# Kernel optimization log

Measured on AMD Instinct MI355X. Metric: run time of the kernel, lower is better.

Reference implementation:

```python
import jax, jax.numpy as jnp
import numpy as np

D = 768      # embed_dim
L = 8        # depth
NH = 4       # num_heads
HD = D // NH # head_dim = 192
GS = 16      # grid size (max_grid_size)
S = GS * GS  # 256 tokens
B = 64
EPS = 1.1920929e-07  # torch.finfo(float32).eps (RMSNorm eps=None)


def rmsnorm(x):
    return x * jax.lax.rsqrt(jnp.mean(x * x, axis=-1, keepdims=True) + EPS)


def householder_Q(vs):
    # sequential chain of Householder reflections: Q <- Q - (2/||v||^2) v (v^T Q)
    def step(Q, v):
        v = v[:, None]
        Q = Q - (2.0 / (jnp.sum(v * v) + 1e-08)) * (v @ (v.T @ Q))
        return Q, None
    Q, _ = jax.lax.scan(step, jnp.eye(vs.shape[1], dtype=vs.dtype), vs)
    return Q


def setup_inputs() -> dict:
    key = jax.random.key(0)
    ks = jax.random.split(key, 16)
    r = lambda k, shape, s=0.02: jax.random.normal(k, shape, jnp.float32) * s
    return dict(
        z_t=jax.random.normal(ks[0], (B, 3, 32, 32), jnp.float32),
        logsnr=jax.random.normal(ks[1], (B,), jnp.float32),
        qkv_w=r(ks[2], (L, D, 3 * D)),
        out_w=r(ks[3], (L, D, D)),
        gate_w=r(ks[4], (L, D, D)), gate_b=jnp.zeros((L, D), jnp.float32),
        mlpg_w=r(ks[5], (L, D, 8 * D)), mlpg_b=jnp.zeros((L, 8 * D), jnp.float32),
        mlpo_w=r(ks[6], (L, 4 * D, D)), mlpo_b=jnp.zeros((L, D), jnp.float32),
        hh_vs=r(ks[7], (L, HD // 2, HD)),
        patch_w=r(ks[8], (20, D)), patch_b=jnp.zeros((D,), jnp.float32),
        head_w=r(ks[9], (D, 12)), head_b=jnp.zeros((12,), jnp.float32),
        sd1_w=r(ks[10], (8, D)), sd1_b=jnp.zeros((D,), jnp.float32),
        sd2_w=r(ks[11], (D, 12)), sd2_b=jnp.zeros((12,), jnp.float32),
        lam_w=r(ks[12], (D, 1)), lam_b=jnp.zeros((1,), jnp.float32),
    )


def reference(z_t, logsnr, qkv_w, out_w, gate_w, gate_b, mlpg_w, mlpg_b,
              mlpo_w, mlpo_b, hh_vs, patch_w, patch_b, head_w, head_b,
              sd1_w, sd1_b, sd2_w, sd2_b, lam_w, lam_b):
    Bn, C, Him, Wim = z_t.shape
    gh = Him // 2
    # patchify 2x2 -> [B, S, 12]
    patches = z_t.reshape(Bn, C, gh, 2, gh, 2).transpose(0, 2, 4, 1, 3, 5).reshape(Bn, S, 12)
    # FourierFeatures(num_bands=4) -> 8-dim sin/cos embedding of logsnr
    bands = 2.0 ** jnp.arange(4, dtype=jnp.float32)
    ang = logsnr[:, None] * bands
    spins = jnp.concatenate([jnp.sin(ang), jnp.cos(ang)], axis=-1)  # [B, 8]
    x = jnp.concatenate([patches, jnp.broadcast_to(spins[:, None, :], (Bn, S, 8))], axis=-1) @ patch_w + patch_b

    # 2D RoPE tables on the 16x16 grid
    yy, xx = jnp.meshgrid(jnp.arange(GS), jnp.arange(GS), indexing='ij')
    coords = jnp.stack([yy.ravel(), xx.ravel()], axis=1).astype(jnp.float32)  # [S, 2]
    dim_half = HD // 2
    inv_freq = 1.0 / 10000.0 ** (jnp.arange(0, dim_half, 2, dtype=jnp.float32) / dim_half)
    fy = coords[:, 0:1] * inv_freq
    fx = coords[:, 1:2] * inv_freq
    emb = jnp.concatenate([fy, fx, fy, fx], axis=-1)  # [S, HD]
    cos, sin = jnp.cos(emb), jnp.sin(emb)

    # local sliding-window mask: euclidean distance on grid < 2.5
    d2 = jnp.sum((coords[:, None, :] - coords[None, :, :]) ** 2, axis=-1)
    local_mask = d2 < 2.5 ** 2  # [S, S]
    is_glob = jnp.array([(i + 1) % 4 == 0 for i in range(L)])
    scale = 1.0 / jnp.sqrt(jnp.float32(HD))

    def layer(x, p):
        qw, ow, gw, gb, mgw, mgb, mow, mob, vs, glob = p
        h = rmsnorm(x)
        q, k, v = jnp.split(h @ qw, 3, axis=-1)
        heads = lambda t: t.reshape(Bn, S, NH, HD).transpose(0, 2, 1, 3)  # [B,H,S,hd]
        q, k, v = heads(q), heads(k), heads(v)
        # RnRoPE: inverse Householder -> rotate -> forward Householder
        Q = householder_Q(vs)
        q, k = q @ Q.T, k @ Q.T
        def rot(t):
            t1, t2 = jnp.split(t, 2, axis=-1)
            return t * cos + jnp.concatenate([-t2, t1], axis=-1) * sin
        q, k = rot(q) @ Q, rot(k) @ Q
        scores = jnp.einsum('bhqd,bhkd->bhqk', q, k) * scale
        keep = local_mask | glob  # global layers attend everywhere
        scores = jnp.where(keep, scores, -1e30)
        attn = jax.nn.softmax(scores, axis=-1) @ v  # [B,H,S,hd]
        attn = attn.transpose(0, 2, 1, 3).reshape(Bn, S, D) @ ow
        gate = jax.nn.sigmoid(attn @ gw + gb)
        x = x + attn * gate
        g, val = jnp.split(rmsnorm(x) @ mgw + mgb, 2, axis=-1)
        x = x + (val * jax.nn.gelu(g, approximate=False)) @ mow + mob
        return x, None

    x, _ = jax.lax.scan(layer, x, (qkv_w, out_w, gate_w, gate_b, mlpg_w, mlpg_b,
                                   mlpo_w, mlpo_b, hh_vs, is_glob))
    x = rmsnorm(x)
    z_pred = x @ head_w + head_b  # [B, S, 12]
    # factorized mode: FourierScaleDecoder scale and lambda head
    scale_f = jnp.exp(jax.nn.silu(spins @ sd1_w + sd1_b) @ sd2_w + sd2_b)  # [B, 12]
    z_pred = z_pred * scale_f[:, None, :]
    l_pred = (jnp.mean(x, axis=1) @ lam_w + lam_b)[:, 0]
    z_img = z_pred.reshape(Bn, gh, gh, 3, 2, 2).transpose(0, 3, 1, 4, 2, 5).reshape(Bn, C, Him, Wim)
    return z_img, l_pred
```

## Files before the change

kernel.cpp:

```cpp
#include <hip/hip_runtime.h>
#include <hip/hip_bf16.h>
#include <math.h>


#define DEV static __device__ __forceinline__

typedef float    f32x4 __attribute__((ext_vector_type(4)));
typedef short    s16x8 __attribute__((ext_vector_type(8)));
typedef unsigned short u16x8 __attribute__((ext_vector_type(8)));
typedef unsigned short u16x4 __attribute__((ext_vector_type(4)));

constexpr int Bb = 64, Ss = 256, Dd = 768, Ll = 8, NHh = 4, HDd = 192;
constexpr int M_TOK = Bb * Ss;
constexpr float EPS_RMS = 1.1920929e-07f;
constexpr float ATT_SCALE = 0.07216878364870322f;
constexpr size_t ARENA_K = (size_t)Bb * NHh * Ss * HDd;

constexpr size_t B_SPINS  = 0;
constexpr size_t B_SCALEF = 2048;
constexpr size_t B_QT     = 5120;
constexpr size_t B_COS    = B_QT + 1179648;
constexpr size_t B_SIN    = B_COS + 196608;
constexpr size_t B_G      = B_SIN + 196608;
constexpr size_t B_T      = B_G + 294912;
constexpr size_t B_AWY    = B_T + 294912;
constexpr size_t B_ROWLAM = B_AWY + 589824;
constexpr size_t B_X      = B_ROWLAM + 65536;
constexpr size_t B_H      = B_X + 50331648;
constexpr size_t B_PROJ   = B_H + 25165824;
constexpr size_t B_WEFFT  = B_PROJ + 25165824;
constexpr size_t B_OUTWT  = B_WEFFT + 28311552;
constexpr size_t B_GATEWT = B_OUTWT + 9437184;
constexpr size_t B_MLPGT  = B_GATEWT + 9437184;
constexpr size_t B_MLPOT  = B_MLPGT + 75497472;
constexpr size_t B_ARENA  = B_MLPOT + 37748736;

DEV float sigmoidf_(float x) { return 1.0f / (1.0f + expf(-x)); }
DEV float geluf_(float g)    { return 0.5f * g * (1.0f + erff(g * 0.7071067811865476f)); }
DEV unsigned short f2bf(float f) {
    union { float f; unsigned u; } a; a.f = f;
    unsigned u = a.u + 0x7fffu + ((a.u >> 16) & 1u);
    return (unsigned short)(u >> 16);
}
DEV float b2f(unsigned short u) {
    union { unsigned u; float f; } a; a.u = ((unsigned)u) << 16; return a.f;
}
DEV void gload16(const void* g, void* l) {
    __builtin_amdgcn_global_load_lds((const __attribute__((address_space(1))) void*)g,
                                     (__attribute__((address_space(3))) void*)l, 16, 0, 0);
}

__global__ void spins_kernel(const float* __restrict__ logsnr, float* __restrict__ spins) {
    int b = threadIdx.x;
    if (b < 64) {
        float v = logsnr[b];
#pragma unroll
        for (int j = 0; j < 4; ++j) {
            float ang = v * (float)(1 << j);
            spins[b * 8 + j]     = sinf(ang);
            spins[b * 8 + 4 + j] = cosf(ang);
        }
    }
}

__global__ void rope_table_kernel(float* __restrict__ cosb, float* __restrict__ sinb) {
    int s = blockIdx.x, j = threadIdx.x;
    int y = s >> 4, x = s & 15;
    int base = j % 96;
    float coord, invf;
    if (base < 48) { invf = expf(-(float)base * (2.0f / 96.0f) * 9.210340371976184f); coord = (float)y; }
    else { int i = base - 48; invf = expf(-(float)i * (2.0f / 96.0f) * 9.210340371976184f); coord = (float)x; }
    float f = coord * invf, sv, cv;
    sincosf(f, &sv, &cv);
    cosb[s * 192 + j] = cv;
    sinb[s * 192 + j] = sv;
}

__global__ __launch_bounds__(256) void hh_gram_kernel(const float* __restrict__ hh_vs,
                                                      float* __restrict__ Gm) {
    __shared__ float Y[96][192];
    int l = blockIdx.x, t = threadIdx.x;
    const float4* src = (const float4*)(hh_vs + (size_t)l * 96 * 192);
    for (int i = t; i < 4608; i += 256) ((float4*)&Y[0][0])[i] = src[i];
    __syncthreads();
    for (int e = t; e < 9216; e += 256) {
        int i = e / 96, j = e - (e / 96) * 96;
        float acc = 0.f;
        for (int d = 0; d < 48; ++d) {
            float4 a = *(const float4*)&Y[i][d * 4];
            float4 b = *(const float4*)&Y[j][d * 4];
            acc += a.x * b.x + a.y * b.y + a.z * b.z + a.w * b.w;
        }
        Gm[(size_t)l * 9216 + e] = acc;
    }
}

__global__ __launch_bounds__(128) void hh_t_kernel(const float* __restrict__ Gm,
                                                   float* __restrict__ Tm) {
    __shared__ float G[96][96];
    __shared__ float T[96][100];
    int l = blockIdx.x, t = threadIdx.x;
    const float* Gl = Gm + (size_t)l * 9216;
    for (int i = t; i < 9216; i += 128) { G[i / 96][i % 96] = Gl[i]; }
    for (int i = t; i < 9600; i += 128) { T[i / 100][i % 100] = 0.f; }
    __syncthreads();
    if (t < 96) T[t][t] = 2.0f / (G[t][t] + 1e-8f);
    __syncthreads();
    for (int j = 1; j < 96; ++j) {
        if (t < j) {
            float cj = 2.0f / (G[j][j] + 1e-8f);
            float dot = 0.f;
            for (int p = t; p < j; ++p) dot += T[t][p] * G[p][j];
            T[t][j] = -cj * dot;
        }
        __syncthreads();
    }
    for (int i = t; i < 9216; i += 128) Tm[(size_t)l * 9216 + i] = T[i / 96][i % 96];
}

__global__ __launch_bounds__(256) void hh_a_kernel(const float* __restrict__ Tm,
                                                   const float* __restrict__ hh_vs,
                                                   float* __restrict__ Am) {
    __shared__ float T[96][100];
    __shared__ float Y[96][192];
    int l = blockIdx.x, t = threadIdx.x;
    const float* Tl = Tm + (size_t)l * 9216;
    const float4* src = (const float4*)(hh_vs + (size_t)l * 96 * 192);
    for (int i = t; i < 9216; i += 256) T[i / 96][i % 96] = Tl[i];
    for (int i = t; i < 4608; i += 256) ((float4*)&Y[0][0])[i] = src[i];
    __syncthreads();
    for (int idx = t; idx < 4608; idx += 256) {
        int i = idx / 48, e0 = (idx % 48) * 4;
        float4 acc = {0.f, 0.f, 0.f, 0.f};
        for (int j = i; j < 96; ++j) {
            float tv = T[i][j];
            float4 y = *(const float4*)&Y[j][e0];
            acc.x += tv * y.x; acc.y += tv * y.y; acc.z += tv * y.z; acc.w += tv * y.w;
        }
        *(float4*)(Am + (size_t)l * 96 * 192 + (size_t)i * 192 + e0) = acc;
    }
}

__global__ __launch_bounds__(256) void hh_p_kernel(const float* __restrict__ hh_vs,
                                                   const float* __restrict__ Am,
                                                   float* __restrict__ qt) {
    __shared__ float Y[96][192];
    __shared__ float A[96][192];
    int l = blockIdx.x, t = threadIdx.x;
    const float4* ys = (const float4*)(hh_vs + (size_t)l * 96 * 192);
    const float4* as = (const float4*)(Am + (size_t)l * 96 * 192);
    for (int i = t; i < 4608; i += 256) { ((float4*)&Y[0][0])[i] = ys[i]; ((float4*)&A[0][0])[i] = as[i]; }
    __syncthreads();
    for (int idx = t; idx < 9216; idx += 256) {
        int d = idx / 48, e0 = (idx % 48) * 4;
        float4 acc = {0.f, 0.f, 0.f, 0.f};
        for (int i = 0; i < 96; ++i) {
            float yv = Y[i][d];
            float4 a = *(const float4*)&A[i][e0];
            acc.x += yv * a.x; acc.y += yv * a.y; acc.z += yv * a.z; acc.w += yv * a.w;
        }
        acc.x = (d == e0 + 0 ? 1.f : 0.f) - acc.x;
        acc.y = (d == e0 + 1 ? 1.f : 0.f) - acc.y;
        acc.z = (d == e0 + 2 ? 1.f : 0.f) - acc.z;
        acc.w = (d == e0 + 3 ? 1.f : 0.f) - acc.w;
        *(float4*)(qt + (size_t)l * 192 * 192 + (size_t)d * 192 + e0) = acc;
    }
}

__global__ __launch_bounds__(256) void fold_kernel(const float* __restrict__ qkv_w,
                                                   const float* __restrict__ qt,
                                                   float* __restrict__ weff) {
    int z = blockIdx.z;
    int l = z >> 3, which = (z >> 2) & 1, head = z & 3;
    const float* A  = qkv_w + (size_t)l * 768 * 2304 + (size_t)which * 768 + head * 192;
    const float* Bq = qt + (size_t)l * 192 * 192;
    float* C        = weff + (size_t)l * 768 * 2304 + (size_t)which * 768 + head * 192;
    int row0 = blockIdx.y * 64, col0 = blockIdx.x * 64;
    __shared__ float As[64][65];
    __shared__ float Bs[64][65];
    int tid = threadIdx.x, tx = tid & 15, ty = tid >> 4;
    float acc[4][4] = {};
    for (int k0 = 0; k0 < 192; k0 += 64) {
        for (int i = tid; i < 1024; i += 256) {
            int r = i >> 4, kq = i & 15;
            float4 va = *(const float4*)(A + (size_t)(row0 + r) * 2304 + k0 + kq * 4);
            As[kq * 4 + 0][r] = va.x; As[kq * 4 + 1][r] = va.y; As[kq * 4 + 2][r] = va.z; As[kq * 4 + 3][r] = va.w;
        }
        for (int i = tid; i < 1024; i += 256) {
            int r = i >> 4, nq = i & 15;
            float4 vb = *(const float4*)(Bq + (size_t)(k0 + r) * 192 + col0 + nq * 4);
            Bs[r][nq * 4 + 0] = vb.x; Bs[r][nq * 4 + 1] = vb.y; Bs[r][nq * 4 + 2] = vb.z; Bs[r][nq * 4 + 3] = vb.w;
        }
        __syncthreads();
        for (int k = 0; k < 64; ++k) {
            float a[4], bb[4];
#pragma unroll
            for (int m = 0; m < 4; ++m) a[m] = As[k][ty * 4 + m];
#pragma unroll
            for (int n = 0; n < 4; ++n) bb[n] = Bs[k][tx * 4 + n];
#pragma unroll
            for (int m = 0; m < 4; ++m)
#pragma unroll
                for (int n = 0; n < 4; ++n) acc[m][n] = fmaf(a[m], bb[n], acc[m][n]);
        }
        __syncthreads();
    }
#pragma unroll
    for (int m = 0; m < 4; ++m)
#pragma unroll
        for (int n = 0; n < 4; ++n)
            C[(size_t)(row0 + ty * 4 + m) * 2304 + col0 + tx * 4 + n] = acc[m][n];
}

__global__ __launch_bounds__(256) void transpose_bf16_kernel(const float* __restrict__ W,
                                                             unsigned short* __restrict__ Wt,
                                                             int K, int N) {
    __shared__ float t[32][33];
    size_t zoff = (size_t)blockIdx.z * K * N;
    const float* Wz = W + zoff;
    unsigned short* Wtz = Wt + zoff;
    int k0 = blockIdx.y * 32, n0 = blockIdx.x * 32;
    int tid = threadIdx.x;
    int tr = tid >> 3, tc = tid & 7;
    float4 v = *(const float4*)(Wz + (size_t)(k0 + tr) * N + n0 + tc * 4);
    t[tr][tc * 4 + 0] = v.x; t[tr][tc * 4 + 1] = v.y; t[tr][tc * 4 + 2] = v.z; t[tr][tc * 4 + 3] = v.w;
    __syncthreads();
    u16x4 o;
    o[0] = f2bf(t[tc * 4 + 0][tr]); o[1] = f2bf(t[tc * 4 + 1][tr]);
    o[2] = f2bf(t[tc * 4 + 2][tr]); o[3] = f2bf(t[tc * 4 + 3][tr]);
    *(u16x4*)(Wtz + (size_t)(n0 + tr) * K + k0 + tc * 4) = o;
}

__global__ __launch_bounds__(256) void patch_embed_kernel(const float* __restrict__ z_t,
                                                          const float* __restrict__ spins,
                                                          const float* __restrict__ patch_w,
                                                          const float* __restrict__ patch_b,
                                                          float* __restrict__ x) {
    int bs = blockIdx.x;
    int b = bs >> 8, s = bs & 255;
    int gy = s >> 4, gx = s & 15;
    __shared__ float in20[20];
    int t = threadIdx.x;
    if (t < 12) {
        int c = t >> 2, py = (t >> 1) & 1, px = t & 1;
        in20[t] = z_t[(((size_t)b * 3 + c) * 32 + (2 * gy + py)) * 32 + (2 * gx + px)];
    } else if (t < 20) {
        in20[t] = spins[b * 8 + (t - 12)];
    }
    __syncthreads();
    for (int d = t; d < 768; d += 256) {
        float acc = patch_b[d];
#pragma unroll
        for (int i = 0; i < 20; ++i) acc += in20[i] * patch_w[i * 768 + d];
        x[(size_t)bs * 768 + d] = acc;
    }
}

__global__ __launch_bounds__(256) void rmsnorm_kernel(const float* __restrict__ x,
                                                      unsigned short* __restrict__ h) {
    int wave = threadIdx.x >> 6, lane = threadIdx.x & 63;
    int row = blockIdx.x * 4 + wave;
    const float* xr = x + (size_t)row * 768 + lane * 12;
    float4 a = *(const float4*)(xr);
    float4 b = *(const float4*)(xr + 4);
    float4 c = *(const float4*)(xr + 8);
    float ss = a.x*a.x + a.y*a.y + a.z*a.z + a.w*a.w
             + b.x*b.x + b.y*b.y + b.z*b.z + b.w*b.w
             + c.x*c.x + c.y*c.y + c.z*c.z + c.w*c.w;
#pragma unroll
    for (int msk = 1; msk < 64; msk <<= 1) ss += __shfl_xor(ss, msk);
    float sc = 1.0f / sqrtf(ss / 768.0f + EPS_RMS);
    unsigned short* hr = h + (size_t)row * 768 + lane * 12;
    u16x4 o0, o1, o2;
    o0[0]=f2bf(a.x*sc); o0[1]=f2bf(a.y*sc); o0[2]=f2bf(a.z*sc); o0[3]=f2bf(a.w*sc);
    o1[0]=f2bf(b.x*sc); o1[1]=f2bf(b.y*sc); o1[2]=f2bf(b.z*sc); o1[3]=f2bf(b.w*sc);
    o2[0]=f2bf(c.x*sc); o2[1]=f2bf(c.y*sc); o2[2]=f2bf(c.z*sc); o2[3]=f2bf(c.w*sc);
    *(u16x4*)(hr) = o0; *(u16x4*)(hr + 4) = o1; *(u16x4*)(hr + 8) = o2;
}

template <int EPI>
__global__ __launch_bounds__(256) void gemm_mfma(const unsigned short* __restrict__ A, int lda,
                                                 const unsigned short* __restrict__ Bt, int ldb,
                                                 unsigned short* __restrict__ Cb, int ldc, int K,
                                                 const float* __restrict__ bias,
                                                 float* __restrict__ Xf,
                                                 const unsigned short* __restrict__ Pb) {
    __shared__ unsigned short As[4096];
    __shared__ unsigned short Bs[4096];
    int tid = threadIdx.x;
    int wave = tid >> 6, lane = tid & 63;
    int row0 = blockIdx.y * 128, col0 = blockIdx.x * 128;
    int wm = wave >> 1, wn = wave & 1;
    f32x4 acc[4][4] = {};

    int srow = lane >> 2;
    int ksw = (((lane & 3) ^ (srow & 3)) * 8);
    int lrow = lane & 15;
    int csw = (((lane >> 4) ^ (lane & 3)) * 8);

    for (int k0 = 0; k0 < K; k0 += 32) {
#pragma unroll
        for (int it = 0; it < 2; ++it) {
            int chunk = it * 4 + wave;
            int r = chunk * 16 + srow;
            gload16(A  + (size_t)(row0 + r) * lda + k0 + ksw, &As[chunk * 512]);
            gload16(Bt + (size_t)(col0 + r) * ldb + k0 + ksw, &Bs[chunk * 512]);
        }
        __syncthreads();
        s16x8 af[4], bf[4];
#pragma unroll
        for (int m = 0; m < 4; ++m)
            af[m] = *(const s16x8*)&As[(wm * 64 + m * 16 + lrow) * 32 + csw];
#pragma unroll
        for (int n = 0; n < 4; ++n)
            bf[n] = *(const s16x8*)&Bs[(wn * 64 + n * 16 + lrow) * 32 + csw];
#pragma unroll
        for (int m = 0; m < 4; ++m)
#pragma unroll
            for (int n = 0; n < 4; ++n)
                acc[m][n] = __builtin_amdgcn_mfma_f32_16x16x32_bf16(af[m], bf[n], acc[m][n], 0, 0, 0);
        __syncthreads();
    }

    int lquad = lane >> 4;
#pragma unroll
    for (int m = 0; m < 4; ++m) {
#pragma unroll
        for (int n = 0; n < 4; ++n) {
#pragma unroll
            for (int r = 0; r < 4; ++r) {
                int i = row0 + wm * 64 + m * 16 + lquad * 4 + r;
                int j = col0 + wn * 64 + n * 16 + lrow;
                float v = acc[m][n][r];
                if (bias) v += bias[j];
                if constexpr (EPI == 0) {
                    Cb[(size_t)i * ldc + j] = f2bf(v);
                } else if constexpr (EPI == 1) {
                    int which = j / 768;
                    int rem = j - which * 768;
                    int head = rem / 192;
                    int hd = rem - head * 192;
                    int b = i >> 8, s = i & 255;
                    if (which == 2) {
                        Cb[2 * ARENA_K + (((size_t)(b * 4 + head)) * 192 + hd) * 256 + s] = f2bf(v);
                    } else {
                        Cb[(size_t)which * ARENA_K + (((size_t)(b * 4 + head)) * 256 + s) * 192 + hd] = f2bf(v);
                    }
                } else if constexpr (EPI == 2) {
                    float p = b2f(Pb[(size_t)i * 768 + j]);
                    Xf[(size_t)i * 768 + j] += p * sigmoidf_(v);
                } else if constexpr (EPI == 4) {
                    Xf[(size_t)i * ldc + j] += v;
                }
            }
        }
    }
}

__global__ __launch_bounds__(256) void gemm_mlp_fused(const unsigned short* __restrict__ A,
                                                      const unsigned short* __restrict__ Bt,
                                                      unsigned short* __restrict__ Hid,
                                                      const float* __restrict__ bias) {
    __shared__ unsigned short As[4096];
    __shared__ unsigned short Bs[4096];
    int tid = threadIdx.x;
    int wave = tid >> 6, lane = tid & 63;
    int row0 = blockIdx.y * 128, col0 = blockIdx.x * 64;
    int wm = wave >> 1, wn = wave & 1;
    f32x4 accg[4][2] = {};
    f32x4 accv[4][2] = {};

    int srow = lane >> 2;
    int ksw = (((lane & 3) ^ (srow & 3)) * 8);
    int lrow = lane & 15;
    int csw = (((lane >> 4) ^ (lane & 3)) * 8);

    const unsigned short* Bg = Bt + (size_t)col0 * 768;
    const unsigned short* Bv = Bt + (size_t)(3072 + col0) * 768;

    for (int k0 = 0; k0 < 768; k0 += 32) {
#pragma unroll
        for (int it = 0; it < 2; ++it) {
            int chunk = it * 4 + wave;
            int r = chunk * 16 + srow;
            gload16(A + (size_t)(row0 + r) * 768 + k0 + ksw, &As[chunk * 512]);
        }
        {
            int r = wave * 16 + srow;
            gload16(Bg + (size_t)r * 768 + k0 + ksw, &Bs[wave * 512]);
            gload16(Bv + (size_t)r * 768 + k0 + ksw, &Bs[2048 + wave * 512]);
        }
        __syncthreads();
        s16x8 af[4], bgf[2], bvf[2];
#pragma unroll
        for (int m = 0; m < 4; ++m)
            af[m] = *(const s16x8*)&As[(wm * 64 + m * 16 + lrow) * 32 + csw];
#pragma unroll
        for (int n = 0; n < 2; ++n) {
            bgf[n] = *(const s16x8*)&Bs[(wn * 32 + n * 16 + lrow) * 32 + csw];
            bvf[n] = *(const s16x8*)&Bs[2048 + (wn * 32 + n * 16 + lrow) * 32 + csw];
        }
#pragma unroll
        for (int m = 0; m < 4; ++m)
#pragma unroll
            for (int n = 0; n < 2; ++n) {
                accg[m][n] = __builtin_amdgcn_mfma_f32_16x16x32_bf16(af[m], bgf[n], accg[m][n], 0, 0, 0);
                accv[m][n] = __builtin_amdgcn_mfma_f32_16x16x32_bf16(af[m], bvf[n], accv[m][n], 0, 0, 0);
            }
        __syncthreads();
    }

    int lquad = lane >> 4;
#pragma unroll
    for (int m = 0; m < 4; ++m) {
#pragma unroll
        for (int n = 0; n < 2; ++n) {
#pragma unroll
            for (int r = 0; r < 4; ++r) {
                int i = row0 + wm * 64 + m * 16 + lquad * 4 + r;
                int j = col0 + wn * 32 + n * 16 + lrow;
                float g = accg[m][n][r] + bias[j];
                float v = accv[m][n][r] + bias[3072 + j];
                Hid[(size_t)i * 3072 + j] = f2bf(v * geluf_(g));
            }
        }
    }
}

__global__ __launch_bounds__(256) void rope_kernel(unsigned short* __restrict__ qk,
                                                   const float* __restrict__ cosb,
                                                   const float* __restrict__ sinb) {
    int gid = blockIdx.x * 256 + threadIdx.x;
    int row = gid / 24, q4 = gid - row * 24;
    int j0 = q4 * 4;
    int s = row & 255;
    unsigned short* p = qk + (size_t)row * 192;
    u16x4 t1 = *(u16x4*)(p + j0);
    u16x4 t2 = *(u16x4*)(p + 96 + j0);
    u16x4 o1, o2;
#pragma unroll
    for (int i = 0; i < 4; ++i) {
        float a = b2f(t1[i]), b = b2f(t2[i]);
        float c1 = cosb[s * 192 + j0 + i],      s1 = sinb[s * 192 + j0 + i];
        float c2 = cosb[s * 192 + 96 + j0 + i], s2 = sinb[s * 192 + 96 + j0 + i];
        o1[i] = f2bf(a * c1 - b * s1);
        o2[i] = f2bf(b * c2 + a * s2);
    }
    *(u16x4*)(p + j0) = o1;
    *(u16x4*)(p + 96 + j0) = o2;
}

__global__ __launch_bounds__(512) void attn_mfma_kernel(const unsigned short* __restrict__ qb_,
                                                        const unsigned short* __restrict__ kb_,
                                                        const unsigned short* __restrict__ vtb_,
                                                        unsigned short* __restrict__ attnb,
                                                        int glob) {
    __shared__ unsigned short Klds[256 * 200];
    __shared__ unsigned short Vlds[192 * 72];
    __shared__ unsigned short Plds[8 * 16 * 72];
    int b = blockIdx.z, hh = blockIdx.y;
    int tid = threadIdx.x;
    int wave = tid >> 6, lane = tid & 63;
    int q0 = blockIdx.x * 128 + wave * 16;
    size_t bh = (size_t)(b * 4 + hh);
    const unsigned short* qb  = qb_  + bh * 49152;
    const unsigned short* kb  = kb_  + bh * 49152;
    const unsigned short* vtb = vtb_ + bh * 49152;

    for (int c = tid; c < 6144; c += 512) {
        int r = c / 24, col = c - (c / 24) * 24;
        *(u16x8*)&Klds[r * 200 + col * 8] = *(const u16x8*)(kb + (size_t)r * 192 + col * 8);
    }
    __syncthreads();

    s16x8 qf[6];
#pragma unroll
    for (int kk = 0; kk < 6; ++kk)
        qf[kk] = *(const s16x8*)(qb + (size_t)(q0 + (lane & 15)) * 192 + kk * 32 + (lane >> 4) * 8);

    f32x4 sc[16];
#pragma unroll
    for (int n = 0; n < 16; ++n) sc[n] = (f32x4){0.f, 0.f, 0.f, 0.f};
#pragma unroll
    for (int kk = 0; kk < 6; ++kk) {
#pragma unroll
        for (int n = 0; n < 16; ++n) {
            s16x8 bf = *(const s16x8*)&Klds[(n * 16 + (lane & 15)) * 200 + kk * 32 + (lane >> 4) * 8];
            sc[n] = __builtin_amdgcn_mfma_f32_16x16x32_bf16(qf[kk], bf, sc[n], 0, 0, 0);
        }
    }

    int lq = (lane >> 4) * 4;
#pragma unroll
    for (int n = 0; n < 16; ++n) {
        int sk = n * 16 + (lane & 15);
        int yk = sk >> 4, xk = sk & 15;
#pragma unroll
        for (int r = 0; r < 4; ++r) {
            int sq = q0 + lq + r;
            int dy = (sq >> 4) - yk, dx = (sq & 15) - xk;
            bool keep = glob || (dy * dy + dx * dx) < 7;
            sc[n][r] = keep ? sc[n][r] * ATT_SCALE : -1e30f;
        }
    }
    float rmax[4], rsum[4];
#pragma unroll
    for (int r = 0; r < 4; ++r) {
        float m = sc[0][r];
#pragma unroll
        for (int n = 1; n < 16; ++n) m = fmaxf(m, sc[n][r]);
#pragma unroll
        for (int msk = 1; msk < 16; msk <<= 1) m = fmaxf(m, __shfl_xor(m, msk));
        rmax[r] = m;
    }
#pragma unroll
    for (int r = 0; r < 4; ++r) {
        float e = 0.f;
#pragma unroll
        for (int n = 0; n < 16; ++n) { float p = expf(sc[n][r] - rmax[r]); sc[n][r] = p; e += p; }
#pragma unroll
        for (int msk = 1; msk < 16; msk <<= 1) e += __shfl_xor(e, msk);
        rsum[r] = 1.0f / e;
    }

    f32x4 o[12];
#pragma unroll
    for (int n = 0; n < 12; ++n) o[n] = (f32x4){0.f, 0.f, 0.f, 0.f};
    unsigned short* Pw = &Plds[wave * 1152];
    for (int kt = 0; kt < 4; ++kt) {
#pragma unroll
        for (int nn = 0; nn < 4; ++nn) {
#pragma unroll
            for (int r = 0; r < 4; ++r)
                Pw[(lq + r) * 72 + nn * 16 + (lane & 15)] = f2bf(sc[kt * 4 + nn][r] * rsum[r]);
        }
        __syncthreads();
        for (int c = tid; c < 1536; c += 512) {
            int r = c >> 3, col = c & 7;
            *(u16x8*)&Vlds[r * 72 + col * 8] = *(const u16x8*)(vtb + (size_t)r * 256 + kt * 64 + col * 8);
        }
        __syncthreads();
        s16x8 af[2];
#pragma unroll
        for (int kk2 = 0; kk2 < 2; ++kk2)
            af[kk2] = *(const s16x8*)&Pw[(lane & 15) * 72 + kk2 * 32 + (lane >> 4) * 8];
#pragma unroll
        for (int n = 0; n < 12; ++n) {
#pragma unroll
            for (int kk2 = 0; kk2 < 2; ++kk2) {
                s16x8 bf = *(const s16x8*)&Vlds[(n * 16 + (lane & 15)) * 72 + kk2 * 32 + (lane >> 4) * 8];
                o[n] = __builtin_amdgcn_mfma_f32_16x16x32_bf16(af[kk2], bf, o[n], 0, 0, 0);
            }
        }
    }
#pragma unroll
    for (int n = 0; n < 12; ++n) {
        int d = n * 16 + (lane & 15);
#pragma unroll
        for (int r = 0; r < 4; ++r) {
            int sq = q0 + lq + r;
            attnb[((size_t)(b * 256 + sq)) * 768 + hh * 192 + d] = f2bf(o[n][r]);
        }
    }
}

__global__ __launch_bounds__(768) void scalef_kernel(const float* __restrict__ spins,
                                                     const float* __restrict__ sd1_w,
                                                     const float* __restrict__ sd1_b,
                                                     const float* __restrict__ sd2_w,
                                                     const float* __restrict__ sd2_b,
                                                     float* __restrict__ scalef) {
    int b = blockIdx.x, t = threadIdx.x;
    __shared__ float hid[768];
    __shared__ float sp[8];
    if (t < 8) sp[t] = spins[b * 8 + t];
    __syncthreads();
    float acc = sd1_b[t];
#pragma unroll
    for (int i = 0; i < 8; ++i) acc += sp[i] * sd1_w[i * 768 + t];
    hid[t] = acc * sigmoidf_(acc);
    __syncthreads();
    if (t < 12) {
        float o = sd2_b[t];
        for (int d = 0; d < 768; ++d) o += hid[d] * sd2_w[d * 12 + t];
        scalef[b * 12 + t] = expf(o);
    }
}

__global__ __launch_bounds__(256) void head_kernel(const unsigned short* __restrict__ xn,
                                                   const float* __restrict__ head_w,
                                                   const float* __restrict__ head_b,
                                                   const float* __restrict__ scalef,
                                                   const float* __restrict__ lam_w,
                                                   float* __restrict__ out,
                                                   float* __restrict__ rowlam) {
    __shared__ float hw[768][13];
    __shared__ float red[4][64][14];
    int t = threadIdx.x, wave = t >> 6, lane = t & 63;
    for (int i = t; i < 768 * 12; i += 256) hw[i / 12][i % 12] = head_w[i];
    for (int i = t; i < 768; i += 256) hw[i][12] = lam_w[i];
    __syncthreads();
    int row_base = blockIdx.x * 64;
    for (int rr = wave; rr < 64; rr += 4) {
        int row = row_base + rr;
        const unsigned short* xr = xn + (size_t)row * 768 + lane * 12;
        float xv[12];
        u16x4 v0 = *(const u16x4*)(xr);
        u16x4 v1 = *(const u16x4*)(xr + 4);
        u16x4 v2 = *(const u16x4*)(xr + 8);
#pragma unroll
        for (int j = 0; j < 4; ++j) { xv[j] = b2f(v0[j]); xv[4 + j] = b2f(v1[j]); xv[8 + j] = b2f(v2[j]); }
        float p[13] = {};
        int d0 = lane * 12;
#pragma unroll
        for (int dd = 0; dd < 12; ++dd) {
            float xvv = xv[dd];
#pragma unroll
            for (int o = 0; o < 12; ++o) p[o] += xvv * hw[d0 + dd][o];
            p[12] += xvv * hw[d0 + dd][12];
        }
#pragma unroll
        for (int o = 0; o < 13; ++o) red[wave][lane][o] = p[o];
        __syncthreads();
        if (lane < 13) {
            float s = 0.f;
            for (int i = 0; i < 64; ++i) s += red[wave][i][lane];
            if (lane < 12) {
                int b = row >> 8, sidx = row & 255;
                float v = (s + head_b[lane]) * scalef[b * 12 + lane];
                int c = lane >> 2, py = (lane >> 1) & 1, px = lane & 1;
                int gy = sidx >> 4, gxx = sidx & 15;
                out[(((size_t)b * 3 + c) * 32 + 2 * gy + py) * 32 + 2 * gxx + px] = v;
            } else {
                rowlam[row] = s;
            }
        }
        __syncthreads();
    }
}

__global__ __launch_bounds__(256) void lpred_kernel(const float* __restrict__ rowlam,
                                                    const float* __restrict__ lam_b,
                                                    float* __restrict__ out) {
    int b = blockIdx.x, t = threadIdx.x;
    __shared__ float red[256];
    red[t] = rowlam[b * 256 + t];
    __syncthreads();
    for (int s2 = 128; s2 > 0; s2 >>= 1) { if (t < s2) red[t] += red[t + s2]; __syncthreads(); }
    if (t == 0) out[196608 + b] = red[0] / 256.0f + lam_b[0];
}

extern "C" void kernel_launch(void* const* d_in, const int* in_sizes, int n_in,
                              void* d_out, int out_size, void* d_ws, size_t ws_size,
                              hipStream_t stream) {
    const float* z_t     = (const float*)d_in[0];
    const float* logsnr  = (const float*)d_in[1];
    const float* qkv_w   = (const float*)d_in[2];
    const float* out_w   = (const float*)d_in[3];
    const float* gate_w  = (const float*)d_in[4];
    const float* gate_b  = (const float*)d_in[5];
    const float* mlpg_w  = (const float*)d_in[6];
    const float* mlpg_b  = (const float*)d_in[7];
    const float* mlpo_w  = (const float*)d_in[8];
    const float* mlpo_b  = (const float*)d_in[9];
    const float* hh_vs   = (const float*)d_in[10];
    const float* patch_w = (const float*)d_in[11];
    const float* patch_b = (const float*)d_in[12];
    const float* head_w  = (const float*)d_in[13];
    const float* head_b  = (const float*)d_in[14];
    const float* sd1_w   = (const float*)d_in[15];
    const float* sd1_b   = (const float*)d_in[16];
    const float* sd2_w   = (const float*)d_in[17];
    const float* sd2_b   = (const float*)d_in[18];
    const float* lam_w   = (const float*)d_in[19];
    const float* lam_b   = (const float*)d_in[20];

    char* wsb = (char*)d_ws;
    float* spins  = (float*)(wsb + B_SPINS);
    float* scalef = (float*)(wsb + B_SCALEF);
    float* qt     = (float*)(wsb + B_QT);
    float* cosb   = (float*)(wsb + B_COS);
    float* sinb   = (float*)(wsb + B_SIN);
    float* Gm     = (float*)(wsb + B_G);
    float* Tm     = (float*)(wsb + B_T);
    float* Am     = (float*)(wsb + B_AWY);
    float* rowlam = (float*)(wsb + B_ROWLAM);
    float* x      = (float*)(wsb + B_X);
    unsigned short* h      = (unsigned short*)(wsb + B_H);
    unsigned short* proj   = (unsigned short*)(wsb + B_PROJ);
    unsigned short* weff_t = (unsigned short*)(wsb + B_WEFFT);
    unsigned short* outw_t = (unsigned short*)(wsb + B_OUTWT);
    unsigned short* gatew_t= (unsigned short*)(wsb + B_GATEWT);
    unsigned short* mlpg_t = (unsigned short*)(wsb + B_MLPGT);
    unsigned short* mlpo_t = (unsigned short*)(wsb + B_MLPOT);
    unsigned short* arena  = (unsigned short*)(wsb + B_ARENA);
    unsigned short* qbuf = arena;
    unsigned short* kbuf = arena + ARENA_K;
    unsigned short* vtbuf = arena + 2 * ARENA_K;
    unsigned short* attnb = arena + 3 * ARENA_K;
    unsigned short* hidden = arena;
    float* weff_f = (float*)(wsb + B_ARENA);
    float* out = (float*)d_out;

    spins_kernel<<<1, 64, 0, stream>>>(logsnr, spins);
    rope_table_kernel<<<256, 192, 0, stream>>>(cosb, sinb);
    hh_gram_kernel<<<8, 256, 0, stream>>>(hh_vs, Gm);
    hh_t_kernel<<<8, 128, 0, stream>>>(Gm, Tm);
    hh_a_kernel<<<8, 256, 0, stream>>>(Tm, hh_vs, Am);
    hh_p_kernel<<<8, 256, 0, stream>>>(hh_vs, Am, qt);
    hipMemcpyAsync(weff_f, qkv_w, (size_t)Ll * Dd * 3 * Dd * sizeof(float),
                   hipMemcpyDeviceToDevice, stream);
    fold_kernel<<<dim3(3, 12, 64), 256, 0, stream>>>(qkv_w, qt, weff_f);
    transpose_bf16_kernel<<<dim3(72, 24, 8), 256, 0, stream>>>(weff_f, weff_t, 768, 2304);
    transpose_bf16_kernel<<<dim3(24, 24, 8), 256, 0, stream>>>(out_w, outw_t, 768, 768);
    transpose_bf16_kernel<<<dim3(24, 24, 8), 256, 0, stream>>>(gate_w, gatew_t, 768, 768);
    transpose_bf16_kernel<<<dim3(192, 24, 8), 256, 0, stream>>>(mlpg_w, mlpg_t, 768, 6144);
    transpose_bf16_kernel<<<dim3(24, 96, 8), 256, 0, stream>>>(mlpo_w, mlpo_t, 3072, 768);
    patch_embed_kernel<<<M_TOK, 256, 0, stream>>>(z_t, spins, patch_w, patch_b, x);

    for (int l = 0; l < Ll; ++l) {
        int glob = ((l + 1) % 4 == 0) ? 1 : 0;
        rmsnorm_kernel<<<4096, 256, 0, stream>>>(x, h);
        gemm_mfma<1><<<dim3(18, 128), 256, 0, stream>>>(h, 768,
            weff_t + (size_t)l * 2304 * 768, 768, arena, 0, 768, nullptr, nullptr, nullptr);
        rope_kernel<<<12288, 256, 0, stream>>>(arena, cosb, sinb);
        attn_mfma_kernel<<<dim3(2, 4, 64), 512, 0, stream>>>(qbuf, kbuf, vtbuf, attnb, glob);
        gemm_mfma<0><<<dim3(6, 128), 256, 0, stream>>>(attnb, 768,
            outw_t + (size_t)l * 768 * 768, 768, proj, 768, 768, nullptr, nullptr, nullptr);
        gemm_mfma<2><<<dim3(6, 128), 256, 0, stream>>>(proj, 768,
            gatew_t + (size_t)l * 768 * 768, 768, nullptr, 768, 768,
            gate_b + (size_t)l * 768, x, proj);
        rmsnorm_kernel<<<4096, 256, 0, stream>>>(x, h);
        gemm_mlp_fused<<<dim3(48, 128), 256, 0, stream>>>(h,
            mlpg_t + (size_t)l * 6144 * 768, hidden, mlpg_b + (size_t)l * 6144);
        gemm_mfma<4><<<dim3(6, 128), 256, 0, stream>>>(hidden, 3072,
            mlpo_t + (size_t)l * 768 * 3072, 3072, nullptr, 768, 3072,
            mlpo_b + (size_t)l * 768, x, nullptr);
    }

    rmsnorm_kernel<<<4096, 256, 0, stream>>>(x, h);
    scalef_kernel<<<64, 768, 0, stream>>>(spins, sd1_w, sd1_b, sd2_w, sd2_b, scalef);
    head_kernel<<<256, 256, 0, stream>>>(h, head_w, head_b, scalef, lam_w, out, rowlam);
    lpred_kernel<<<64, 256, 0, stream>>>(rowlam, lam_b, out);
}
```

Measured before the change: 6.410 ms.

## Fuse RoPE into attention loads and fold QKV weights directly to transposed bf16

Removes the standalone RoPE pass by applying the rotary rotation while loading K into LDS and Q fragments inside the attention kernel. This saves a full read-modify-write of Q and K per layer. The cost is redundant rotation work, since each of the two q-blocks per head re-rotates K, plus extra cos/sin loads. The setup path is also reshaped: the fold kernel now writes transposed bf16 weights directly, replacing the device-to-device memcpy and the full fp32 transpose, and only the V slice is transposed separately. The Householder T matrix is stored transposed so the triangular-solve inner loop reads shared memory with better access patterns.

```diff
diff --git a/kernel.cpp b/kernel.cpp
--- a/kernel.cpp
+++ b/kernel.cpp
@@ -98,42 +98,41 @@
 __global__ __launch_bounds__(128) void hh_t_kernel(const float* __restrict__ Gm,
                                                    float* __restrict__ Tm) {
     __shared__ float G[96][96];
-    __shared__ float T[96][100];
+    __shared__ float Tt[96][96];
     int l = blockIdx.x, t = threadIdx.x;
     const float* Gl = Gm + (size_t)l * 9216;
-    for (int i = t; i < 9216; i += 128) { G[i / 96][i % 96] = Gl[i]; }
-    for (int i = t; i < 9600; i += 128) { T[i / 100][i % 100] = 0.f; }
-    __syncthreads();
-    if (t < 96) T[t][t] = 2.0f / (G[t][t] + 1e-8f);
+    for (int i = t; i < 9216; i += 128) { ((float*)G)[i] = Gl[i]; ((float*)Tt)[i] = 0.f; }
+    __syncthreads();
+    if (t < 96) Tt[t][t] = 2.0f / (G[t][t] + 1e-8f);
     __syncthreads();
     for (int j = 1; j < 96; ++j) {
         if (t < j) {
             float cj = 2.0f / (G[j][j] + 1e-8f);
             float dot = 0.f;
-            for (int p = t; p < j; ++p) dot += T[t][p] * G[p][j];
-            T[t][j] = -cj * dot;
-        }
-        __syncthreads();
-    }
-    for (int i = t; i < 9216; i += 128) Tm[(size_t)l * 9216 + i] = T[i / 96][i % 96];
+            for (int p = t; p < j; ++p) dot += Tt[p][t] * G[p][j];
+            Tt[j][t] = -cj * dot;
+        }
+        __syncthreads();
+    }
+    for (int i = t; i < 9216; i += 128) Tm[(size_t)l * 9216 + i] = ((float*)Tt)[i];
 }
 
 __global__ __launch_bounds__(256) void hh_a_kernel(const float* __restrict__ Tm,
                                                    const float* __restrict__ hh_vs,
                                                    float* __restrict__ Am) {
-    __shared__ float T[96][100];
+    __shared__ float T[96][96];
     __shared__ float Y[96][192];
     int l = blockIdx.x, t = threadIdx.x;
     const float* Tl = Tm + (size_t)l * 9216;
     const float4* src = (const float4*)(hh_vs + (size_t)l * 96 * 192);
-    for (int i = t; i < 9216; i += 256) T[i / 96][i % 96] = Tl[i];
+    for (int i = t; i < 9216; i += 256) ((float*)T)[i] = Tl[i];
     for (int i = t; i < 4608; i += 256) ((float4*)&Y[0][0])[i] = src[i];
     __syncthreads();
     for (int idx = t; idx < 4608; idx += 256) {
         int i = idx / 48, e0 = (idx % 48) * 4;
         float4 acc = {0.f, 0.f, 0.f, 0.f};
         for (int j = i; j < 96; ++j) {
-            float tv = T[i][j];
+            float tv = T[j][i];
             float4 y = *(const float4*)&Y[j][e0];
             acc.x += tv * y.x; acc.y += tv * y.y; acc.z += tv * y.z; acc.w += tv * y.w;
         }
@@ -167,14 +166,14 @@
     }
 }
 
-__global__ __launch_bounds__(256) void fold_kernel(const float* __restrict__ qkv_w,
-                                                   const float* __restrict__ qt,
-                                                   float* __restrict__ weff) {
+__global__ __launch_bounds__(256) void fold_bf16t(const float* __restrict__ qkv_w,
+                                                  const float* __restrict__ qt,
+                                                  unsigned short* __restrict__ weff_t) {
     int z = blockIdx.z;
     int l = z >> 3, which = (z >> 2) & 1, head = z & 3;
     const float* A  = qkv_w + (size_t)l * 768 * 2304 + (size_t)which * 768 + head * 192;
     const float* Bq = qt + (size_t)l * 192 * 192;
-    float* C        = weff + (size_t)l * 768 * 2304 + (size_t)which * 768 + head * 192;
+    unsigned short* C = weff_t + (size_t)l * 2304 * 768 + ((size_t)which * 768 + head * 192) * 768;
     int row0 = blockIdx.y * 64, col0 = blockIdx.x * 64;
     __shared__ float As[64][65];
     __shared__ float Bs[64][65];
@@ -205,30 +204,39 @@
         }
         __syncthreads();
     }
+    float (*Tr)[65] = (float(*)[65])As;
 #pragma unroll
     for (int m = 0; m < 4; ++m)
 #pragma unroll
-        for (int n = 0; n < 4; ++n)
-            C[(size_t)(row0 + ty * 4 + m) * 2304 + col0 + tx * 4 + n] = acc[m][n];
+        for (int n = 0; n < 4; ++n) Tr[tx * 4 + n][ty * 4 + m] = acc[m][n];
+    __syncthreads();
+    int nl = tid >> 2, kc = (tid & 3) * 16;
+#pragma unroll
+    for (int q4 = 0; q4 < 4; ++q4) {
+        u16x4 o;
+#pragma unroll
+        for (int ii = 0; ii < 4; ++ii) o[ii] = f2bf(Tr[nl][kc + q4 * 4 + ii]);
+        *(u16x4*)(C + (size_t)(col0 + nl) * 768 + row0 + kc + q4 * 4) = o;
+    }
 }
 
 __global__ __launch_bounds__(256) void transpose_bf16_kernel(const float* __restrict__ W,
+                                                             int ldw, size_t zsrc,
                                                              unsigned short* __restrict__ Wt,
-                                                             int K, int N) {
+                                                             int ldwt, size_t zdst) {
     __shared__ float t[32][33];
-    size_t zoff = (size_t)blockIdx.z * K * N;
-    const float* Wz = W + zoff;
-    unsigned short* Wtz = Wt + zoff;
+    const float* Wz = W + (size_t)blockIdx.z * zsrc;
+    unsigned short* Wtz = Wt + (size_t)blockIdx.z * zdst;
     int k0 = blockIdx.y * 32, n0 = blockIdx.x * 32;
     int tid = threadIdx.x;
     int tr = tid >> 3, tc = tid & 7;
-    float4 v = *(const float4*)(Wz + (size_t)(k0 + tr) * N + n0 + tc * 4);
+    float4 v = *(const float4*)(Wz + (size_t)(k0 + tr) * ldw + n0 + tc * 4);
     t[tr][tc * 4 + 0] = v.x; t[tr][tc * 4 + 1] = v.y; t[tr][tc * 4 + 2] = v.z; t[tr][tc * 4 + 3] = v.w;
     __syncthreads();
     u16x4 o;
     o[0] = f2bf(t[tc * 4 + 0][tr]); o[1] = f2bf(t[tc * 4 + 1][tr]);
     o[2] = f2bf(t[tc * 4 + 2][tr]); o[3] = f2bf(t[tc * 4 + 3][tr]);
-    *(u16x4*)(Wtz + (size_t)(n0 + tr) * K + k0 + tc * 4) = o;
+    *(u16x4*)(Wtz + (size_t)(n0 + tr) * ldwt + k0 + tc * 4) = o;
 }
 
 __global__ __launch_bounds__(256) void patch_embed_kernel(const float* __restrict__ z_t,
@@ -427,33 +435,12 @@
     }
 }
 
-__global__ __launch_bounds__(256) void rope_kernel(unsigned short* __restrict__ qk,
-                                                   const float* __restrict__ cosb,
-                                                   const float* __restrict__ sinb) {
-    int gid = blockIdx.x * 256 + threadIdx.x;
-    int row = gid / 24, q4 = gid - row * 24;
-    int j0 = q4 * 4;
-    int s = row & 255;
-    unsigned short* p = qk + (size_t)row * 192;
-    u16x4 t1 = *(u16x4*)(p + j0);
-    u16x4 t2 = *(u16x4*)(p + 96 + j0);
-    u16x4 o1, o2;
-#pragma unroll
-    for (int i = 0; i < 4; ++i) {
-        float a = b2f(t1[i]), b = b2f(t2[i]);
-        float c1 = cosb[s * 192 + j0 + i],      s1 = sinb[s * 192 + j0 + i];
-        float c2 = cosb[s * 192 + 96 + j0 + i], s2 = sinb[s * 192 + 96 + j0 + i];
-        o1[i] = f2bf(a * c1 - b * s1);
-        o2[i] = f2bf(b * c2 + a * s2);
-    }
-    *(u16x4*)(p + j0) = o1;
-    *(u16x4*)(p + 96 + j0) = o2;
-}
-
 __global__ __launch_bounds__(512) void attn_mfma_kernel(const unsigned short* __restrict__ qb_,
                                                         const unsigned short* __restrict__ kb_,
                                                         const unsigned short* __restrict__ vtb_,
                                                         unsigned short* __restrict__ attnb,
+                                                        const float* __restrict__ cosb,
+                                                        const float* __restrict__ sinb,
                                                         int glob) {
     __shared__ unsigned short Klds[256 * 200];
     __shared__ unsigned short Vlds[192 * 72];
@@ -469,14 +456,41 @@
 
     for (int c = tid; c < 6144; c += 512) {
         int r = c / 24, col = c - (c / 24) * 24;
-        *(u16x8*)&Klds[r * 200 + col * 8] = *(const u16x8*)(kb + (size_t)r * 192 + col * 8);
+        int j0 = col * 8;
+        int jp = j0 < 96 ? j0 + 96 : j0 - 96;
+        float sgn = j0 < 96 ? -1.f : 1.f;
+        u16x8 a = *(const u16x8*)(kb + (size_t)r * 192 + j0);
+        u16x8 p = *(const u16x8*)(kb + (size_t)r * 192 + jp);
+        const float* cr = cosb + r * 192 + j0;
+        const float* sr = sinb + r * 192 + j0;
+        u16x8 o;
+#pragma unroll
+        for (int i = 0; i < 8; ++i)
+            o[i] = f2bf(b2f(a[i]) * cr[i] + sgn * b2f(p[i]) * sr[i]);
+        *(u16x8*)&Klds[r * 200 + j0] = o;
     }
     __syncthreads();
 
     s16x8 qf[6];
-#pragma unroll
-    for (int kk = 0; kk < 6; ++kk)
-        qf[kk] = *(const s16x8*)(qb + (size_t)(q0 + (lane & 15)) * 192 + kk * 32 + (lane >> 4) * 8);
+    {
+        int sq = q0 + (lane & 15);
+        const unsigned short* qrow = qb + (size_t)sq * 192;
+        const float* cr = cosb + sq * 192;
+        const float* sr = sinb + sq * 192;
+#pragma unroll
+        for (int kk = 0; kk < 6; ++kk) {
+            int ck = kk * 32 + (lane >> 4) * 8;
+            int cp = ck < 96 ? ck + 96 : ck - 96;
+            float sgn = ck < 96 ? -1.f : 1.f;
+            u16x8 a = *(const u16x8*)(qrow + ck);
+            u16x8 p = *(const u16x8*)(qrow + cp);
+            s16x8 o;
+#pragma unroll
+            for (int i = 0; i < 8; ++i)
+                o[i] = (short)f2bf(b2f(a[i]) * cr[ck + i] + sgn * b2f(p[i]) * sr[ck + i]);
+            qf[kk] = o;
+        }
+    }
 
     f32x4 sc[16];
 #pragma unroll
@@ -699,7 +713,6 @@
     unsigned short* vtbuf = arena + 2 * ARENA_K;
     unsigned short* attnb = arena + 3 * ARENA_K;
     unsigned short* hidden = arena;
-    float* weff_f = (float*)(wsb + B_ARENA);
     float* out = (float*)d_out;
 
     spins_kernel<<<1, 64, 0, stream>>>(logsnr, spins);
@@ -708,14 +721,17 @@
     hh_t_kernel<<<8, 128, 0, stream>>>(Gm, Tm);
     hh_a_kernel<<<8, 256, 0, stream>>>(Tm, hh_vs, Am);
     hh_p_kernel<<<8, 256, 0, stream>>>(hh_vs, Am, qt);
-    hipMemcpyAsync(weff_f, qkv_w, (size_t)Ll * Dd * 3 * Dd * sizeof(float),
-                   hipMemcpyDeviceToDevice, stream);
-    fold_kernel<<<dim3(3, 12, 64), 256, 0, stream>>>(qkv_w, qt, weff_f);
-    transpose_bf16_kernel<<<dim3(72, 24, 8), 256, 0, stream>>>(weff_f, weff_t, 768, 2304);
-    transpose_bf16_kernel<<<dim3(24, 24, 8), 256, 0, stream>>>(out_w, outw_t, 768, 768);
-    transpose_bf16_kernel<<<dim3(24, 24, 8), 256, 0, stream>>>(gate_w, gatew_t, 768, 768);
-    transpose_bf16_kernel<<<dim3(192, 24, 8), 256, 0, stream>>>(mlpg_w, mlpg_t, 768, 6144);
-    transpose_bf16_kernel<<<dim3(24, 96, 8), 256, 0, stream>>>(mlpo_w, mlpo_t, 3072, 768);
+    fold_bf16t<<<dim3(3, 12, 64), 256, 0, stream>>>(qkv_w, qt, weff_t);
+    transpose_bf16_kernel<<<dim3(24, 24, 8), 256, 0, stream>>>(qkv_w + 1536, 2304,
+        (size_t)768 * 2304, weff_t + (size_t)1536 * 768, 768, (size_t)2304 * 768);
+    transpose_bf16_kernel<<<dim3(24, 24, 8), 256, 0, stream>>>(out_w, 768,
+        (size_t)768 * 768, outw_t, 768, (size_t)768 * 768);
+    transpose_bf16_kernel<<<dim3(24, 24, 8), 256, 0, stream>>>(gate_w, 768,
+        (size_t)768 * 768, gatew_t, 768, (size_t)768 * 768);
+    transpose_bf16_kernel<<<dim3(192, 24, 8), 256, 0, stream>>>(mlpg_w, 6144,
+        (size_t)768 * 6144, mlpg_t, 768, (size_t)6144 * 768);
+    transpose_bf16_kernel<<<dim3(24, 96, 8), 256, 0, stream>>>(mlpo_w, 768,
+        (size_t)3072 * 768, mlpo_t, 3072, (size_t)768 * 3072);
     patch_embed_kernel<<<M_TOK, 256, 0, stream>>>(z_t, spins, patch_w, patch_b, x);
 
     for (int l = 0; l < Ll; ++l) {
@@ -723,8 +739,8 @@
         rmsnorm_kernel<<<4096, 256, 0, stream>>>(x, h);
         gemm_mfma<1><<<dim3(18, 128), 256, 0, stream>>>(h, 768,
             weff_t + (size_t)l * 2304 * 768, 768, arena, 0, 768, nullptr, nullptr, nullptr);
-        rope_kernel<<<12288, 256, 0, stream>>>(arena, cosb, sinb);
-        attn_mfma_kernel<<<dim3(2, 4, 64), 512, 0, stream>>>(qbuf, kbuf, vtbuf, attnb, glob);
+        attn_mfma_kernel<<<dim3(2, 4, 64), 512, 0, stream>>>(qbuf, kbuf, vtbuf, attnb,
+            cosb, sinb, glob);
         gemm_mfma<0><<<dim3(6, 128), 256, 0, stream>>>(attnb, 768,
             outw_t + (size_t)l * 768 * 768, 768, proj, 768, 768, nullptr, nullptr, nullptr);
         gemm_mfma<2><<<dim3(6, 128), 256, 0, stream>>>(proj, 768,
```

After: 6.320 ms. No clear change (-1.4%).
